# Kernel optimization log

Hardware: AMD Instinct MI355X
Metric: run time of the kernel (lower is better)

Reference implementation:

```python
import jax, jax.numpy as jnp
import numpy as np

B = 2048        # patients (segments)
K = 4           # images per patient
C = 1280        # backbone_out (tf_efficientnet_b0)
PAIRS = K * (K - 1) // 2  # torch.combinations -> 6
NCLS = 1
N_DROP = 5


def setup_inputs() -> dict:
    key = jax.random.key(0)
    ks = jax.random.split(key, 8)
    x = jax.random.normal(ks[0], (B * K, C), jnp.float32)  # detached backbone features
    ids2 = jnp.repeat(jnp.arange(B, dtype=jnp.int32), PAIRS)  # segment id per pair
    Wc = jax.random.normal(ks[1], (C, C, 2), jnp.float32) * 0.02  # Conv1d(C,C,k=2) weight
    bc = jnp.zeros((C,), jnp.float32)
    W0 = jax.random.normal(ks[2], (NCLS, C), jnp.float32) * 0.02
    b0 = jnp.zeros((NCLS,), jnp.float32)
    W1 = jax.random.normal(ks[3], (1, C), jnp.float32) * 0.02
    b1 = jnp.zeros((1,), jnp.float32)
    W2 = jax.random.normal(ks[4], (1, C), jnp.float32) * 0.02
    b2 = jnp.zeros((1,), jnp.float32)
    return dict(x=x, ids2=ids2, Wc=Wc, bc=bc, W0=W0, b0=b0, W1=W1, b1=b1, W2=W2, b2=b2)


def reference(x, ids2, Wc, bc, W0, b0, W1, b1, W2, b2):
    # --- pair combinations within each patient group of K images ---
    ii, jj = np.triu_indices(K, 1)               # static [PAIRS]
    xg = x.reshape(B, K, C)
    xa = xg[:, ii].reshape(B * PAIRS, C)         # first element of each pair
    xb = xg[:, jj].reshape(B * PAIRS, C)         # second element
    # Conv1d(C, C, kernel=2) over the length-2 pair sequence + ReLU
    xc = jax.nn.relu(xa @ Wc[:, :, 0].T + xb @ Wc[:, :, 1].T + bc)  # [P, C]

    # --- 5 fixed dropout masks (p=0.5, train-mode scaling) ---
    masks = jax.random.bernoulli(jax.random.key(42), 0.5,
                                 (N_DROP, xc.shape[0], C)).astype(xc.dtype) * 2.0
    xd = xc[None] * masks                        # [D, P, C]

    cnt = jax.ops.segment_sum(jnp.ones_like(ids2, dtype=xc.dtype),
                              ids2, num_segments=B)  # [B], == PAIRS

    def agg(W, b):
        # head -> scalar mean over classes -> segment-mean over pairs -> mean over dropouts
        z = (jnp.einsum('dpc,oc->dpo', xd, W) + b).mean(-1)          # [D, P]
        s = jax.vmap(lambda u: jax.ops.segment_sum(u, ids2, num_segments=B))(z)
        return (s / cnt).mean(0)                                      # [B]

    logits = agg(W0, b0)
    logits1 = agg(W1, b1)
    logits2 = agg(W2, b2)
    return jnp.stack([logits, logits1, logits2], axis=1)  # [B, 3]
```

## Files before the change

### kernel.cpp

```cpp
#include <hip/hip_runtime.h>


typedef __attribute__((ext_vector_type(8))) short short8;
typedef __attribute__((ext_vector_type(4))) float f32x4;

#define PLANE 15728640u
#define KS2   (0x1BD11BDAu ^ 42u)

__device__ __forceinline__ unsigned short f2bf(float f) {
  unsigned int u = __builtin_bit_cast(unsigned int, f);
  u = (u + 0x7FFFu + ((u >> 16) & 1u)) >> 16;
  return (unsigned short)u;
}
__device__ __forceinline__ float bf2f(unsigned short h) {
  unsigned int u = ((unsigned int)h) << 16;
  return __builtin_bit_cast(float, u);
}

__global__ void init_out(float* __restrict__ out, const float* __restrict__ b0,
                         const float* __restrict__ b1, const float* __restrict__ b2) {
  int i = blockIdx.x * 256 + threadIdx.x;
  if (i < 2048 * 3) {
    int h = i % 3;
    out[i] = (h == 0) ? b0[0] : ((h == 1) ? b1[0] : b2[0]);
  }
}

__global__ void conv_x(const float* __restrict__ x, unsigned short* __restrict__ xb) {
  int i = (blockIdx.x * 256 + threadIdx.x) * 4;
  float4 v = *(const float4*)(x + i);
  ushort4 o;
  o.x = f2bf(v.x); o.y = f2bf(v.y); o.z = f2bf(v.z); o.w = f2bf(v.w);
  *(ushort4*)(xb + i) = o;
}

__global__ void conv_w(const float* __restrict__ Wc, unsigned short* __restrict__ Wb) {
  int idx = blockIdx.x * 256 + threadIdx.x;
  int n = idx / 2560;
  int k = idx - n * 2560;
  int side = (k >= 1280) ? 1 : 0;
  int cin = k - side * 1280;
  Wb[idx] = f2bf(Wc[n * 2560 + cin * 2 + side]);
}

__device__ __forceinline__ unsigned int rotl(unsigned int x, int r) {
  return __builtin_amdgcn_alignbit(x, x, 32 - r);
}
__device__ __forceinline__ unsigned int tf_msb(unsigned int x1) {
  unsigned int x0 = x1;
  x1 = rotl(x1, 13) ^ x0;
#define TF_R(r) { x0 += x1; x1 = rotl(x1, (r)) ^ x0; }
  TF_R(15) TF_R(26) TF_R(6)
  x0 += 42u; x1 += KS2 + 1u;
  TF_R(17) TF_R(29) TF_R(16) TF_R(24)
  x0 += KS2; x1 += 2u;
  TF_R(13) TF_R(15) TF_R(26) TF_R(6)
  x1 += 42u + 3u;
  TF_R(17) TF_R(29) TF_R(16) TF_R(24)
  x0 += 42u; x1 += KS2 + 4u;
  TF_R(13) TF_R(15) TF_R(26) TF_R(6)
  x0 += KS2; x1 += 5u;
#undef TF_R
  return (x0 ^ x1) >> 31;
}

#define GL_LDS(g, l) __builtin_amdgcn_global_load_lds( \
    (const __attribute__((address_space(1))) unsigned int*)(g), \
    (__attribute__((address_space(3))) unsigned int*)(l), 16, 0, 0)

__global__ __launch_bounds__(256) void gemm_relu_dot(
    const unsigned short* __restrict__ Xb,
    const unsigned short* __restrict__ Wb,
    const float* __restrict__ bc,
    const float* __restrict__ W0, const float* __restrict__ W1,
    const float* __restrict__ W2, float* __restrict__ out)
{
  __shared__ unsigned short sA[128 * 32];
  __shared__ unsigned short sB[128 * 32];
  __shared__ unsigned int zLDS[8 * 256];
  __shared__ float rowsumA[128 * 3];
  __shared__ float rowsumB[128 * 3];

  const int t = threadIdx.x;
  const int mblk = blockIdx.x % 96;
  const int nblk = blockIdx.x / 96;
  const int p0 = mblk * 128, n0 = nblk * 128;
  const int lane = t & 63, w = t >> 6;
  const int wr = w >> 1, wc = w & 1;
  const int q = lane & 3;
  const int rl = lane >> 2;
  const int mrow = lane & 15;
  const int koff = (lane >> 4) * 8;
  const int mq = (lane >> 4) * 4;
  const int nn = lane & 15;

  int rA[2], rB[2], rN[2];
#pragma unroll
  for (int i = 0; i < 2; i++) {
    const int row = w * 32 + i * 16 + rl;
    const int pg = p0 + row;
    const int bA = pg / 6, pr = pg - bA * 6;
    rA[i] = bA * 4 + ((0x211000 >> (4 * pr)) & 7);
    rB[i] = bA * 4 + ((0x332321 >> (4 * pr)) & 7);
    rN[i] = n0 + row;
  }
  unsigned short* ldsA0 = sA + (w * 32 + 0) * 32;
  unsigned short* ldsA1 = sA + (w * 32 + 16) * 32;
  unsigned short* ldsB0 = sB + (w * 32 + 0) * 32;
  unsigned short* ldsB1 = sB + (w * 32 + 16) * 32;
  const unsigned short* gA0s0 = Xb + rA[0] * 1280 + q * 8;
  const unsigned short* gA1s0 = Xb + rA[1] * 1280 + q * 8;
  const unsigned short* gA0s1 = Xb + rB[0] * 1280 + q * 8;
  const unsigned short* gA1s1 = Xb + rB[1] * 1280 + q * 8;
  const unsigned short* gB0 = Wb + rN[0] * 2560 + q * 8;
  const unsigned short* gB1 = Wb + rN[1] * 2560 + q * 8;

  f32x4 acc[4][4];
#pragma unroll
  for (int i = 0; i < 4; i++)
#pragma unroll
    for (int j = 0; j < 4; j++) acc[i][j] = (f32x4){0.f, 0.f, 0.f, 0.f};

  const unsigned int tb =
      (unsigned int)((p0 + wr * 64 + mq) * 1280 + n0 + wc * 64 + nn) + 42u;

#define KSTEP(Ga0, Ga1, kb, kg)                                              \
  {                                                                          \
    __syncthreads();                                                         \
    GL_LDS(Ga0 + (kb), ldsA0);                                               \
    GL_LDS(Ga1 + (kb), ldsA1);                                               \
    GL_LDS(gB0 + (kg), ldsB0);                                               \
    GL_LDS(gB1 + (kg), ldsB1);                                               \
    __syncthreads();                                                         \
    short8 af[4], bfr[4];                                                    \
    _Pragma("unroll")                                                        \
    for (int i = 0; i < 4; i++)                                              \
      af[i] = *(const short8*)(sA + (wr * 64 + i * 16 + mrow) * 32 + koff);  \
    _Pragma("unroll")                                                        \
    for (int j = 0; j < 4; j++)                                              \
      bfr[j] = *(const short8*)(sB + (wc * 64 + j * 16 + mrow) * 32 + koff); \
    _Pragma("unroll")                                                        \
    for (int i = 0; i < 4; i++)                                              \
      _Pragma("unroll")                                                      \
      for (int j = 0; j < 4; j++)                                            \
        acc[i][j] = __builtin_amdgcn_mfma_f32_16x16x32_bf16(af[i], bfr[j],   \
                                                            acc[i][j], 0, 0, 0); \
  }

#define CELL_RNG(it)                                                         \
  {                                                                          \
    const int idx = (it);                                                    \
    const unsigned int b = tb +                                              \
        (unsigned int)((((idx >> 4) * 16 + (idx & 3)) * 1280) +              \
                       (((idx >> 2) & 3) * 16));                             \
    const unsigned int z5 = tf_msb(b) + tf_msb(b + PLANE) +                  \
                            tf_msb(b + 2u * PLANE) + tf_msb(b + 3u * PLANE) +\
                            tf_msb(b + 4u * PLANE);                          \
    zacc |= z5 << (4 * sub);                                                 \
  }

  for (int c8 = 0; c8 < 5; c8++) {
    unsigned int zacc = 0;
    for (int sub = 0; sub < 8; sub++) {
      const int it = c8 * 8 + sub;
      KSTEP(gA0s0, gA1s0, it * 32, it * 32);
      CELL_RNG(it);
    }
    zLDS[c8 * 256 + t] = zacc;
  }
  for (int c8 = 5; c8 < 8; c8++) {
    unsigned int zacc = 0;
    for (int sub = 0; sub < 8; sub++) {
      const int it = c8 * 8 + sub;
      KSTEP(gA0s1, gA1s1, (it - 40) * 32, it * 32);
      CELL_RNG(it);
    }
    zLDS[c8 * 256 + t] = zacc;
  }
  for (int c8 = 8; c8 < 10; c8++) {
    for (int sub = 0; sub < 8; sub++) {
      const int it = c8 * 8 + sub;
      KSTEP(gA0s1, gA1s1, (it - 40) * 32, it * 32);
    }
  }
#undef KSTEP
#undef CELL_RNG

  unsigned int zq[8];
#pragma unroll
  for (int c = 0; c < 8; c++) zq[c] = zLDS[c * 256 + t];

  float w0v[4], w1v[4], w2v[4], bcv[4];
#pragma unroll
  for (int j = 0; j < 4; j++) {
    const int n = n0 + wc * 64 + j * 16 + nn;
    w0v[j] = W0[n]; w1v[j] = W1[n]; w2v[j] = W2[n]; bcv[j] = bc[n];
  }

  float* const dst = (wc == 0) ? rowsumA : rowsumB;
#pragma unroll
  for (int i = 0; i < 4; i++) {
#pragma unroll
    for (int rg = 0; rg < 4; rg++) {
      float s0 = 0.f, s1 = 0.f, s2 = 0.f;
#pragma unroll
      for (int j = 0; j < 4; j++) {
        const int idx = i * 16 + j * 4 + rg;
        const unsigned int z5 = (zq[idx >> 3] >> (4 * (idx & 7))) & 7u;
        float v = acc[i][j][rg] + bcv[j];
        v = v > 0.f ? v : 0.f;
        const float tx = v * (float)(5 - (int)z5);
        s0 += tx * w0v[j]; s1 += tx * w1v[j]; s2 += tx * w2v[j];
      }
#pragma unroll
      for (int off = 1; off < 16; off <<= 1) {
        s0 += __shfl_xor(s0, off);
        s1 += __shfl_xor(s1, off);
        s2 += __shfl_xor(s2, off);
      }
      if (nn == 0) {
        const int row = wr * 64 + i * 16 + mq + rg;
        dst[row * 3 + 0] = s0; dst[row * 3 + 1] = s1; dst[row * 3 + 2] = s2;
      }
    }
  }
  __syncthreads();

  if (t < 128) {
    const int pr = p0 + t;
    const int rem = pr % 6;
    if (t == 0 || rem == 0) {
      int nrows = 6 - rem;
      if (nrows > 128 - t) nrows = 128 - t;
      float a0 = 0.f, a1 = 0.f, a2 = 0.f;
      for (int k2 = 0; k2 < nrows; k2++) {
        a0 += rowsumA[(t + k2) * 3 + 0] + rowsumB[(t + k2) * 3 + 0];
        a1 += rowsumA[(t + k2) * 3 + 1] + rowsumB[(t + k2) * 3 + 1];
        a2 += rowsumA[(t + k2) * 3 + 2] + rowsumB[(t + k2) * 3 + 2];
      }
      const int pat = pr / 6;
      atomicAdd(&out[pat * 3 + 0], a0 * (1.0f / 15.0f));
      atomicAdd(&out[pat * 3 + 1], a1 * (1.0f / 15.0f));
      atomicAdd(&out[pat * 3 + 2], a2 * (1.0f / 15.0f));
    }
  }
}

extern "C" void kernel_launch(void* const* d_in, const int* in_sizes, int n_in,
                              void* d_out, int out_size, void* d_ws, size_t ws_size,
                              hipStream_t stream) {
  const float* x  = (const float*)d_in[0];
  const float* Wc = (const float*)d_in[2];
  const float* bc = (const float*)d_in[3];
  const float* W0 = (const float*)d_in[4];
  const float* b0 = (const float*)d_in[5];
  const float* W1 = (const float*)d_in[6];
  const float* b1 = (const float*)d_in[7];
  const float* W2 = (const float*)d_in[8];
  const float* b2 = (const float*)d_in[9];
  float* out = (float*)d_out;

  char* ws = (char*)d_ws;
  unsigned short* xb = (unsigned short*)ws;
  unsigned short* Wb = (unsigned short*)(ws + 20971520);

  init_out<<<24, 256, 0, stream>>>(out, b0, b1, b2);
  conv_x<<<10240, 256, 0, stream>>>(x, xb);
  conv_w<<<12800, 256, 0, stream>>>(Wc, Wb);
  gemm_relu_dot<<<960, 256, 0, stream>>>(xb, Wb, bc, W0, W1, W2, out);
}
```

Measured before the change: 315.9 us.

## Double-buffer GEMM LDS tiles with async prefetch and merge prep kernels

```diff
diff --git a/kernel.cpp b/kernel.cpp
--- a/kernel.cpp
+++ b/kernel.cpp
@@ -17,30 +17,33 @@
   return __builtin_bit_cast(float, u);
 }
 
-__global__ void init_out(float* __restrict__ out, const float* __restrict__ b0,
-                         const float* __restrict__ b1, const float* __restrict__ b2) {
-  int i = blockIdx.x * 256 + threadIdx.x;
-  if (i < 2048 * 3) {
-    int h = i % 3;
-    out[i] = (h == 0) ? b0[0] : ((h == 1) ? b1[0] : b2[0]);
-  }
-}
-
-__global__ void conv_x(const float* __restrict__ x, unsigned short* __restrict__ xb) {
-  int i = (blockIdx.x * 256 + threadIdx.x) * 4;
-  float4 v = *(const float4*)(x + i);
-  ushort4 o;
-  o.x = f2bf(v.x); o.y = f2bf(v.y); o.z = f2bf(v.z); o.w = f2bf(v.w);
-  *(ushort4*)(xb + i) = o;
-}
-
-__global__ void conv_w(const float* __restrict__ Wc, unsigned short* __restrict__ Wb) {
-  int idx = blockIdx.x * 256 + threadIdx.x;
-  int n = idx / 2560;
-  int k = idx - n * 2560;
-  int side = (k >= 1280) ? 1 : 0;
-  int cin = k - side * 1280;
-  Wb[idx] = f2bf(Wc[n * 2560 + cin * 2 + side]);
+__global__ __launch_bounds__(256) void prep(
+    const float* __restrict__ x, unsigned short* __restrict__ xb,
+    const float* __restrict__ Wc, unsigned short* __restrict__ Wb,
+    const float* __restrict__ b0, const float* __restrict__ b1,
+    const float* __restrict__ b2, float* __restrict__ out) {
+  const int bid = blockIdx.x;
+  const int t = threadIdx.x;
+  if (bid < 10240) {
+    const int i = (bid * 256 + t) * 4;
+    float4 v = *(const float4*)(x + i);
+    ushort4 o;
+    o.x = f2bf(v.x); o.y = f2bf(v.y); o.z = f2bf(v.z); o.w = f2bf(v.w);
+    *(ushort4*)(xb + i) = o;
+  } else if (bid < 23040) {
+    const int idx = (bid - 10240) * 256 + t;
+    const int n = idx / 2560;
+    const int k = idx - n * 2560;
+    const int side = (k >= 1280) ? 1 : 0;
+    const int cin = k - side * 1280;
+    Wb[idx] = f2bf(Wc[n * 2560 + cin * 2 + side]);
+  } else {
+    const int i = (bid - 23040) * 256 + t;
+    if (i < 2048 * 3) {
+      const int h = i % 3;
+      out[i] = (h == 0) ? b0[0] : ((h == 1) ? b1[0] : b2[0]);
+    }
+  }
 }
 
 __device__ __forceinline__ unsigned int rotl(unsigned int x, int r) {
@@ -75,8 +78,8 @@
     const float* __restrict__ W0, const float* __restrict__ W1,
     const float* __restrict__ W2, float* __restrict__ out)
 {
-  __shared__ unsigned short sA[128 * 32];
-  __shared__ unsigned short sB[128 * 32];
+  __shared__ unsigned short sA[2 * 128 * 32];
+  __shared__ unsigned short sB[2 * 128 * 32];
   __shared__ unsigned int zLDS[8 * 256];
   __shared__ float rowsumA[128 * 3];
   __shared__ float rowsumB[128 * 3];
@@ -104,16 +107,16 @@
     rB[i] = bA * 4 + ((0x332321 >> (4 * pr)) & 7);
     rN[i] = n0 + row;
   }
-  unsigned short* ldsA0 = sA + (w * 32 + 0) * 32;
-  unsigned short* ldsA1 = sA + (w * 32 + 16) * 32;
-  unsigned short* ldsB0 = sB + (w * 32 + 0) * 32;
-  unsigned short* ldsB1 = sB + (w * 32 + 16) * 32;
-  const unsigned short* gA0s0 = Xb + rA[0] * 1280 + q * 8;
-  const unsigned short* gA1s0 = Xb + rA[1] * 1280 + q * 8;
-  const unsigned short* gA0s1 = Xb + rB[0] * 1280 + q * 8;
-  const unsigned short* gA1s1 = Xb + rB[1] * 1280 + q * 8;
-  const unsigned short* gB0 = Wb + rN[0] * 2560 + q * 8;
-  const unsigned short* gB1 = Wb + rN[1] * 2560 + q * 8;
+  unsigned short* const ldsA0 = sA + (w * 32 + 0) * 32;
+  unsigned short* const ldsA1 = sA + (w * 32 + 16) * 32;
+  unsigned short* const ldsB0 = sB + (w * 32 + 0) * 32;
+  unsigned short* const ldsB1 = sB + (w * 32 + 16) * 32;
+  const unsigned short* const gA0s0 = Xb + rA[0] * 1280 + q * 8;
+  const unsigned short* const gA1s0 = Xb + rA[1] * 1280 + q * 8;
+  const unsigned short* const gA0s1 = Xb + rB[0] * 1280 + q * 8;
+  const unsigned short* const gA1s1 = Xb + rB[1] * 1280 + q * 8;
+  const unsigned short* const gB0 = Wb + rN[0] * 2560 + q * 8;
+  const unsigned short* const gB1 = Wb + rN[1] * 2560 + q * 8;
 
   f32x4 acc[4][4];
 #pragma unroll
@@ -124,21 +127,35 @@
   const unsigned int tb =
       (unsigned int)((p0 + wr * 64 + mq) * 1280 + n0 + wc * 64 + nn) + 42u;
 
-#define KSTEP(Ga0, Ga1, kb, kg)                                              \
+#define PF(nxt, bb)                                                          \
   {                                                                          \
-    __syncthreads();                                                         \
-    GL_LDS(Ga0 + (kb), ldsA0);                                               \
-    GL_LDS(Ga1 + (kb), ldsA1);                                               \
-    GL_LDS(gB0 + (kg), ldsB0);                                               \
-    GL_LDS(gB1 + (kg), ldsB1);                                               \
+    const int _n = (nxt);                                                    \
+    if (_n < 80) {                                                           \
+      const int _s1 = (_n >= 40);                                            \
+      const unsigned short* _a0 = _s1 ? gA0s1 : gA0s0;                       \
+      const unsigned short* _a1 = _s1 ? gA1s1 : gA1s0;                       \
+      const int _kb = (_s1 ? (_n - 40) : _n) * 32;                           \
+      const int _kg = _n * 32;                                               \
+      GL_LDS(_a0 + _kb, ldsA0 + (bb) * 4096);                                \
+      GL_LDS(_a1 + _kb, ldsA1 + (bb) * 4096);                                \
+      GL_LDS(gB0 + _kg, ldsB0 + (bb) * 4096);                                \
+      GL_LDS(gB1 + _kg, ldsB1 + (bb) * 4096);                                \
+    }                                                                        \
+  }
+
+#define KSTEP(it, bb)                                                        \
+  {                                                                          \
     __syncthreads();                                                         \
     short8 af[4], bfr[4];                                                    \
     _Pragma("unroll")                                                        \
     for (int i = 0; i < 4; i++)                                              \
-      af[i] = *(const short8*)(sA + (wr * 64 + i * 16 + mrow) * 32 + koff);  \
+      af[i] = *(const short8*)(sA + (bb) * 4096 +                            \
+                               (wr * 64 + i * 16 + mrow) * 32 + koff);       \
     _Pragma("unroll")                                                        \
     for (int j = 0; j < 4; j++)                                              \
-      bfr[j] = *(const short8*)(sB + (wc * 64 + j * 16 + mrow) * 32 + koff); \
+      bfr[j] = *(const short8*)(sB + (bb) * 4096 +                           \
+                                (wc * 64 + j * 16 + mrow) * 32 + koff);      \
+    PF((it) + 1, ((bb) ^ 1));                                                \
     _Pragma("unroll")                                                        \
     for (int i = 0; i < 4; i++)                                              \
       _Pragma("unroll")                                                      \
@@ -159,31 +176,27 @@
     zacc |= z5 << (4 * sub);                                                 \
   }
 
-  for (int c8 = 0; c8 < 5; c8++) {
+  PF(0, 0);
+
+  for (int c8 = 0; c8 < 8; c8++) {
     unsigned int zacc = 0;
+#pragma unroll
     for (int sub = 0; sub < 8; sub++) {
       const int it = c8 * 8 + sub;
-      KSTEP(gA0s0, gA1s0, it * 32, it * 32);
+      KSTEP(it, (sub & 1));
       CELL_RNG(it);
     }
     zLDS[c8 * 256 + t] = zacc;
   }
-  for (int c8 = 5; c8 < 8; c8++) {
-    unsigned int zacc = 0;
+  for (int c8 = 8; c8 < 10; c8++) {
+#pragma unroll
     for (int sub = 0; sub < 8; sub++) {
       const int it = c8 * 8 + sub;
-      KSTEP(gA0s1, gA1s1, (it - 40) * 32, it * 32);
-      CELL_RNG(it);
-    }
-    zLDS[c8 * 256 + t] = zacc;
-  }
-  for (int c8 = 8; c8 < 10; c8++) {
-    for (int sub = 0; sub < 8; sub++) {
-      const int it = c8 * 8 + sub;
-      KSTEP(gA0s1, gA1s1, (it - 40) * 32, it * 32);
+      KSTEP(it, (sub & 1));
     }
   }
 #undef KSTEP
+#undef PF
 #undef CELL_RNG
 
   unsigned int zq[8];
@@ -264,8 +277,6 @@
   unsigned short* xb = (unsigned short*)ws;
   unsigned short* Wb = (unsigned short*)(ws + 20971520);
 
-  init_out<<<24, 256, 0, stream>>>(out, b0, b1, b2);
-  conv_x<<<10240, 256, 0, stream>>>(x, xb);
-  conv_w<<<12800, 256, 0, stream>>>(Wc, Wb);
+  prep<<<23064, 256, 0, stream>>>(x, xb, Wc, Wb, b0, b1, b2, out);
   gemm_relu_dot<<<960, 256, 0, stream>>>(xb, Wb, bc, W0, W1, W2, out);
 }
```

Measured after the change: 314.2 us. No clear change (-0.5%).
